# Kernel optimization log

Hardware: AMD Instinct MI355X
Metric: run time of the kernel (lower is better)

The kernel has to match this reference:

```python
import jax, jax.numpy as jnp
import numpy as np

N_GRAPHS = 1000
P = 300                 # nodes per ring graph
N = N_GRAPHS * P        # 300000 nodes
IN_DIM = 2
HID = 128
OUT_DIM = 2


def _ring_edges():
    idx = jnp.arange(N)
    g = idx // P
    pos = idx % P
    nxt = g * P + (pos + 1) % P
    src = jnp.concatenate([idx, nxt])
    dst = jnp.concatenate([nxt, idx])
    return jnp.stack([src, dst]), g


def setup_inputs() -> dict:
    key = jax.random.key(0)
    ks = jax.random.split(key, 11)
    edge_index, batch = _ring_edges()
    x = jax.random.normal(ks[0], (N, IN_DIM), jnp.float32)

    def glorot(k, fan_in, fan_out):
        lim = np.sqrt(6.0 / (fan_in + fan_out)).astype(np.float32)
        return jax.random.uniform(k, (fan_in, fan_out), jnp.float32, -lim, lim)

    return {
        "x": x,
        "edge_index": edge_index,
        "batch": batch,
        "W1": glorot(ks[1], IN_DIM, HID), "b1": jnp.zeros((HID,), jnp.float32),
        "W2": glorot(ks[2], HID, HID),    "b2": jnp.zeros((HID,), jnp.float32),
        "W3": glorot(ks[3], HID, HID),    "b3": jnp.zeros((HID,), jnp.float32),
        "fw1": glorot(ks[4], HID, HID),   "fb1": jnp.zeros((HID,), jnp.float32),
        "fw2": glorot(ks[5], HID, OUT_DIM), "fb2": jnp.zeros((OUT_DIM,), jnp.float32),
    }


def _gcn_conv(x, W, b, src, dst, norm):
    h = x @ W                              # [N, out]
    msg = h[src] * norm[:, None]           # gather + per-edge scale
    agg = jax.ops.segment_sum(msg, dst, num_segments=N)  # scatter-add
    return agg + b


def reference(x, edge_index, batch, W1, b1, W2, b2, W3, b3, fw1, fb1, fw2, fb2):
    loop = jnp.arange(N)
    src = jnp.concatenate([edge_index[0], loop])
    dst = jnp.concatenate([edge_index[1], loop])
    deg = jax.ops.segment_sum(jnp.ones_like(dst, jnp.float32), dst, num_segments=N)
    dis = jax.lax.rsqrt(deg)               # deg >= 1 due to self-loops
    norm = dis[src] * dis[dst]             # per-edge normalization

    h = jax.nn.relu(_gcn_conv(x, W1, b1, src, dst, norm))
    h = jax.nn.relu(_gcn_conv(h, W2, b2, src, dst, norm))
    h = jax.nn.relu(_gcn_conv(h, W3, b3, src, dst, norm))

    # global mean pool per graph
    sums = jax.ops.segment_sum(h, batch, num_segments=N_GRAPHS)
    cnts = jax.ops.segment_sum(jnp.ones((N,), jnp.float32), batch, num_segments=N_GRAPHS)
    pooled = sums / cnts[:, None]

    out = jax.nn.relu(pooled @ fw1 + fb1)
    out = out @ fw2 + fb2
    return out
```

## Files before the change

### kernel.cpp

```cpp
#include <hip/hip_runtime.h>
#include <hip/hip_bf16.h>
#include <stdint.h>

#define P    300
#define HID  128
#define NG   1000
#define NTL  19

typedef __attribute__((ext_vector_type(8))) short bf16x8;
typedef __attribute__((ext_vector_type(4))) float f32x4;

__device__ short g_wsw[2 * HID * HID];

__device__ __forceinline__ short f2bf(float f) {
    union { float f; uint32_t u; } v; v.f = f;
    uint32_t r = v.u + 0x7fffu + ((v.u >> 16) & 1u);
    return (short)(r >> 16);
}
__device__ __forceinline__ float bf2f(short s) {
    union { uint32_t u; float f; } v; v.u = ((uint32_t)(uint16_t)s) << 16;
    return v.f;
}
__device__ __forceinline__ uint32_t pkbf2(float a, float b) {
    union { __hip_bfloat162 h; uint32_t u; } cv;
    cv.h = __float22bfloat162_rn(float2{a, b});
    return cv.u;
}
__device__ __forceinline__ float unpk(int v, int ft) {
    return bf2f((short)(ft ? (((uint32_t)v) >> 16) : (v & 0xffff)));
}

__global__ __launch_bounds__(256) void k_prep(const float* __restrict__ W2,
                                              const float* __restrict__ W3) {
    int b = blockIdx.x;
    const bool perm = (b < 8);
    const float* W = perm ? W2 : W3;
    short* dst = g_wsw + (perm ? 0 : HID * HID);
    int t    = (b & 7) * 256 + threadIdx.x;
    int fkey = t >> 4;
    int kc   = t & 15;
    int fsrc;
    if (perm) {
        int u = fkey >> 5, ft = (fkey >> 4) & 1, l = fkey & 15;
        fsrc = u * 32 + 2 * l + ft;
    } else fsrc = fkey;
    bf16x8 o;
    #pragma unroll
    for (int j = 0; j < 8; ++j)
        o[j] = f2bf(W[(kc * 8 + j) * HID + fsrc]);
    *(bf16x8*)&dst[(fkey * 16 + (kc ^ (fkey & 15))) * 8] = o;
}

__device__ __forceinline__ void avg_epi(const float* G, float vp0, float vn3,
                                        float b, float* o) {
    o[0] = (vp0  + G[0] + G[1]) * (1.0f / 3.0f) + b;
    o[1] = (G[0] + G[1] + G[2]) * (1.0f / 3.0f) + b;
    o[2] = (G[1] + G[2] + G[3]) * (1.0f / 3.0f) + b;
    o[3] = (G[2] + G[3] + vn3 ) * (1.0f / 3.0f) + b;
    #pragma unroll
    for (int i = 0; i < 4; ++i) o[i] = o[i] > 0.f ? o[i] : 0.f;
}

template<int POOL>
__device__ __forceinline__ void run_pass(short* __restrict__ buf,
                                         const short* __restrict__ wbase,
                                         const float* __restrict__ bias,
                                         float* __restrict__ pool, int tid) {
    const int lane = tid & 63, wv = tid >> 6, q = lane >> 4, lm = lane & 15;
    const int ftg0 = wv * 2;
    bf16x8 wf[2][4];
    #pragma unroll
    for (int ft = 0; ft < 2; ++ft) {
        int fkey = (ftg0 + ft) * 16 + lm;
        #pragma unroll
        for (int kk = 0; kk < 4; ++kk)
            wf[ft][kk] = *(const bf16x8*)&wbase[(fkey * 16 + ((4 * kk + q) ^ lm)) * 8];
    }
    float biaf[2];
    #pragma unroll
    for (int ft = 0; ft < 2; ++ft)
        biaf[ft] = POOL ? bias[(ftg0 + ft) * 16 + lm] : bias[wv * 32 + 2 * lm + ft];
    const int sA = (q == 0) ? (48 + lm) : (lane - 16);
    const int sB = (lane + 16) & 63;
    const int fpair = wv * 32 + 2 * lm;
    const int kcs = fpair >> 3, offs = fpair & 7;

    float psum[2] = {0.f, 0.f};

    auto mfma_tile = [&](int t, f32x4* G) {
        const short* tb = buf + t * 2048;
        G[0] = f32x4{0.f, 0.f, 0.f, 0.f};
        G[1] = f32x4{0.f, 0.f, 0.f, 0.f};
        #pragma unroll
        for (int kk = 0; kk < 4; ++kk) {
            bf16x8 af = *(const bf16x8*)&tb[(lm * 16 + ((4 * kk + q) ^ lm)) * 8];
            G[0] = __builtin_amdgcn_mfma_f32_16x16x32_bf16(af, wf[0][kk], G[0], 0, 0, 0);
            G[1] = __builtin_amdgcn_mfma_f32_16x16x32_bf16(af, wf[1][kk], G[1], 0, 0, 0);
        }
    };
    auto store_rows = [&](int T, float (&o)[2][4]) {
        #pragma unroll
        for (int i = 0; i < 4; ++i) {
            int node = T * 16 + q * 4 + i;
            *(uint32_t*)&buf[(node * 16 + (kcs ^ (node & 15))) * 8 + offs] =
                pkbf2(o[0][i], o[1][i]);
        }
    };
    auto accum = [&](float (&o)[2][4]) {
        #pragma unroll
        for (int ft = 0; ft < 2; ++ft)
            psum[ft] += o[ft][0] + o[ft][1] + o[ft][2] + o[ft][3];
    };

    float c15[2];
    auto epi_mid = [&](const f32x4 (&E)[2], uint32_t uN0, float (&o)[2][4]) {
        uint32_t uE3 = pkbf2(E[0][3], E[1][3]);
        uint32_t uE0 = pkbf2(E[0][0], E[1][0]);
        int vA = __shfl((int)uE3, sA, 64);
        int vB = __shfl((int)uE0, sB, 64);
        int vC = __shfl((int)uN0, lm, 64);
        #pragma unroll
        for (int ft = 0; ft < 2; ++ft) {
            float bpA = unpk(vA, ft);
            float vp0 = (q == 0) ? c15[ft] : bpA;
            float vn3 = (q == 3) ? unpk(vC, ft) : unpk(vB, ft);
            avg_epi((const float*)&E[ft], vp0, vn3, biaf[ft], o[ft]);
            c15[ft] = bpA;
        }
    };

    f32x4 GH[10][2];
    f32x4 GL[9][2];

    #pragma unroll
    for (int k = 0; k < 9; ++k) mfma_tile(10 + k, GH[k]);
    mfma_tile(0, GH[9]);
    if (!POOL) __syncthreads();

    #pragma unroll
    for (int i = 0; i < 9; ++i) {
        mfma_tile(9 - i, GL[i]);
        if (i == 0) {
            int v = __shfl((int)pkbf2(GL[0][0][3], GL[0][1][3]), 48 + lm, 64);
            c15[0] = unpk(v, 0); c15[1] = unpk(v, 1);
        }
        if (i < 8) {
            float o[2][4];
            uint32_t uN0 = pkbf2(GH[i + 1][0][0], GH[i + 1][1][0]);
            epi_mid(GH[i], uN0, o);
            if (POOL) accum(o); else store_rows(10 + i, o);
        } else {
            float o18[2][4];
            uint32_t uE3 = pkbf2(GH[8][0][3], GH[8][1][3]);
            uint32_t uE0 = pkbf2(GH[8][0][0], GH[8][1][0]);
            uint32_t uZ0 = pkbf2(GH[9][0][0], GH[9][1][0]);
            int vA = __shfl((int)uE3, sA, 64);
            int vB = __shfl((int)uE0, sB, 64);
            int vZ = __shfl((int)uZ0, lm, 64);
            #pragma unroll
            for (int ft = 0; ft < 2; ++ft) {
                float bpA = unpk(vA, ft);
                float vp0 = (q == 0) ? c15[ft] : bpA;
                float vn3 = (q == 2) ? unpk(vZ, ft) : unpk(vB, ft);
                avg_epi((const float*)&GH[8][ft], vp0, vn3, biaf[ft], o18[ft]);
            }
            if (q < 3) { if (POOL) accum(o18); else store_rows(18, o18); }
            float o0[2][4];
            uint32_t uF3 = pkbf2(GH[9][0][3], GH[9][1][3]);
            int vA0 = __shfl((int)uF3, (lane - 16) & 63, 64);
            int vB0 = __shfl((int)uZ0, sB, 64);
            int vP  = __shfl((int)uE3, 32 + lm, 64);
            uint32_t uG1 = pkbf2(GL[8][0][0], GL[8][1][0]);
            int vN = __shfl((int)uG1, lm, 64);
            #pragma unroll
            for (int ft = 0; ft < 2; ++ft) {
                float vp0 = (q == 0) ? unpk(vP, ft) : unpk(vA0, ft);
                float vn3 = (q == 3) ? unpk(vN, ft) : unpk(vB0, ft);
                avg_epi((const float*)&GH[9][ft], vp0, vn3, biaf[ft], o0[ft]);
            }
            if (POOL) accum(o0); else store_rows(0, o0);
        }
    }
    if (!POOL) __syncthreads();

    {
        int v = __shfl((int)pkbf2(GH[9][0][3], GH[9][1][3]), 48 + lm, 64);
        c15[0] = unpk(v, 0); c15[1] = unpk(v, 1);
    }
    #pragma unroll
    for (int T = 1; T <= 9; ++T) {
        float o[2][4];
        uint32_t uN0 = (T < 9) ? pkbf2(GL[8 - T][0][0], GL[8 - T][1][0])
                               : pkbf2(GH[0][0][0], GH[0][1][0]);
        epi_mid(GL[9 - T], uN0, o);
        if (POOL) accum(o); else store_rows(T, o);
    }

    if (POOL) {
        #pragma unroll
        for (int ft = 0; ft < 2; ++ft) {
            psum[ft] += __shfl_xor(psum[ft], 16, 64);
            psum[ft] += __shfl_xor(psum[ft], 32, 64);
        }
        if (q == 0) {
            pool[ftg0 * 16 + lm]      = psum[0];
            pool[ftg0 * 16 + 16 + lm] = psum[1];
        }
    }
}

__global__ __launch_bounds__(256, 2) void k_graph(
        const float* __restrict__ x,
        const float* __restrict__ W1,  const float* __restrict__ b1,
        const float* __restrict__ b2v, const float* __restrict__ b3v,
        const float* __restrict__ fw1, const float* __restrict__ fb1,
        const float* __restrict__ fw2, const float* __restrict__ fb2,
        float* __restrict__ out) {
    __shared__ __align__(16) short buf[304 * HID];
    __shared__ __align__(16) float scr[640];
    float* xs    = scr;
    float* pool  = scr;
    float* parts = scr + 128;
    float* s1    = scr + 384;

    const int g = blockIdx.x, tid = threadIdx.x;

    if (tid < 150) *(float4*)&xs[tid * 4] = *(const float4*)&x[g * 600 + tid * 4];
    __syncthreads();

    {
        const int kc1 = tid & 15;
        const int n0  = tid >> 4;
        float w1x[8], w1y[8], b1v[8];
        #pragma unroll
        for (int j = 0; j < 8; ++j) {
            w1x[j] = W1[kc1 * 8 + j];
            w1y[j] = W1[HID + kc1 * 8 + j];
            b1v[j] = b1[kc1 * 8 + j];
        }
        #pragma unroll
        for (int it = 0; it < NTL; ++it) {
            int node = it * 16 + n0;
            uint32_t w[4] = {0u, 0u, 0u, 0u};
            if (node < P) {
                int prev = (node == 0)     ? P - 1 : node - 1;
                int next = (node == P - 1) ? 0     : node + 1;
                float2 xp = *(const float2*)&xs[2 * prev];
                float2 xc = *(const float2*)&xs[2 * node];
                float2 xn = *(const float2*)&xs[2 * next];
                float ax = (xp.x + xc.x + xn.x) * (1.f / 3.f);
                float ay = (xp.y + xc.y + xn.y) * (1.f / 3.f);
                #pragma unroll
                for (int jj = 0; jj < 4; ++jj) {
                    float va = ax * w1x[2*jj]   + ay * w1y[2*jj]   + b1v[2*jj];
                    float vb = ax * w1x[2*jj+1] + ay * w1y[2*jj+1] + b1v[2*jj+1];
                    va = va > 0.f ? va : 0.f;
                    vb = vb > 0.f ? vb : 0.f;
                    w[jj] = pkbf2(va, vb);
                }
            }
            *(uint4*)&buf[(node * 16 + (kc1 ^ (node & 15))) * 8] =
                uint4{w[0], w[1], w[2], w[3]};
        }
    }
    __syncthreads();

    run_pass<0>(buf, g_wsw,             b2v, pool, tid);
    __syncthreads();
    run_pass<1>(buf, g_wsw + HID * HID, b3v, pool, tid);
    __syncthreads();

    {
        int f = tid & 127, half = tid >> 7;
        float p = 0.f;
        const float* fw1c = fw1 + f;
        #pragma unroll 4
        for (int k = half * 64; k < half * 64 + 64; ++k)
            p += pool[k] * fw1c[k * 128];
        parts[half * 128 + f] = p;
    }
    __syncthreads();
    if (tid < 128) {
        float o1 = fb1[tid] + (parts[tid] + parts[128 + tid]) * (1.0f / 300.0f);
        s1[tid] = o1 > 0.f ? o1 : 0.f;
    }
    __syncthreads();
    if (tid < 128) {
        int o = tid >> 6, ln = tid & 63;
        float v = s1[ln] * fw2[ln * 2 + o] + s1[ln + 64] * fw2[(ln + 64) * 2 + o];
        #pragma unroll
        for (int off = 1; off <= 32; off <<= 1)
            v += __shfl_xor(v, off, 64);
        if (ln == 0) out[g * 2 + o] = v + fb2[o];
    }
}

extern "C" void kernel_launch(void* const* d_in, const int* in_sizes, int n_in,
                              void* d_out, int out_size, void* d_ws, size_t ws_size,
                              hipStream_t stream) {
    const float* x   = (const float*)d_in[0];
    const float* W1  = (const float*)d_in[3];
    const float* b1  = (const float*)d_in[4];
    const float* W2  = (const float*)d_in[5];
    const float* b2  = (const float*)d_in[6];
    const float* W3  = (const float*)d_in[7];
    const float* b3  = (const float*)d_in[8];
    const float* fw1 = (const float*)d_in[9];
    const float* fb1 = (const float*)d_in[10];
    const float* fw2 = (const float*)d_in[11];
    const float* fb2 = (const float*)d_in[12];
    float* out = (float*)d_out;

    k_prep <<<dim3(16), dim3(256), 0, stream>>>(W2, W3);
    k_graph<<<dim3(NG), dim3(256), 0, stream>>>(x, W1, b1, b2, b3,
                                                fw1, fb1, fw2, fb2, out);
}
```

Measured before the change: 123.3 us.

## Replace cross-lane shuffle neighbor exchange with small shift-matrix MFMAs

The ring-neighbor averaging epilogue used to move boundary rows between lanes with several __shfl calls per tile and bf16 unpacking. It now packs every tile's accumulator to bf16 once and feeds the packed values to 16x16x16 MFMAs against constant shift/selection matrices, which bring the cross-row (and wrap-around) neighbor values into each lane's accumulator. This moves the lane exchange from LDS-backed shuffles onto the matrix units. In exchange it adds extra MFMAs per tile and a 19x2 array of packed bf16 tiles that raises register pressure, which may cause spills or lower occupancy.

```diff
diff --git a/kernel.cpp b/kernel.cpp
--- a/kernel.cpp
+++ b/kernel.cpp
@@ -8,6 +8,7 @@
 #define NTL  19
 
 typedef __attribute__((ext_vector_type(8))) short bf16x8;
+typedef __attribute__((ext_vector_type(4))) short bf16x4;
 typedef __attribute__((ext_vector_type(4))) float f32x4;
 
 __device__ short g_wsw[2 * HID * HID];
@@ -17,17 +18,19 @@
     uint32_t r = v.u + 0x7fffu + ((v.u >> 16) & 1u);
     return (short)(r >> 16);
 }
-__device__ __forceinline__ float bf2f(short s) {
-    union { uint32_t u; float f; } v; v.u = ((uint32_t)(uint16_t)s) << 16;
-    return v.f;
-}
 __device__ __forceinline__ uint32_t pkbf2(float a, float b) {
     union { __hip_bfloat162 h; uint32_t u; } cv;
     cv.h = __float22bfloat162_rn(float2{a, b});
     return cv.u;
 }
-__device__ __forceinline__ float unpk(int v, int ft) {
-    return bf2f((short)(ft ? (((uint32_t)v) >> 16) : (v & 0xffff)));
+
+__device__ __forceinline__ f32x4 mfma16(bf16x4 a, bf16x4 b, f32x4 c) {
+#if __has_builtin(__builtin_amdgcn_mfma_f32_16x16x16bf16_1k)
+    return __builtin_amdgcn_mfma_f32_16x16x16bf16_1k(a, b, c, 0, 0, 0);
+#else
+    asm("v_mfma_f32_16x16x16_bf16 %0, %1, %2, %0" : "+v"(c) : "v"(a), "v"(b));
+    return c;
+#endif
 }
 
 __global__ __launch_bounds__(256) void k_prep(const float* __restrict__ W2,
@@ -51,16 +54,6 @@
     *(bf16x8*)&dst[(fkey * 16 + (kc ^ (fkey & 15))) * 8] = o;
 }
 
-__device__ __forceinline__ void avg_epi(const float* G, float vp0, float vn3,
-                                        float b, float* o) {
-    o[0] = (vp0  + G[0] + G[1]) * (1.0f / 3.0f) + b;
-    o[1] = (G[0] + G[1] + G[2]) * (1.0f / 3.0f) + b;
-    o[2] = (G[1] + G[2] + G[3]) * (1.0f / 3.0f) + b;
-    o[3] = (G[2] + G[3] + vn3 ) * (1.0f / 3.0f) + b;
-    #pragma unroll
-    for (int i = 0; i < 4; ++i) o[i] = o[i] > 0.f ? o[i] : 0.f;
-}
-
 template<int POOL>
 __device__ __forceinline__ void run_pass(short* __restrict__ buf,
                                          const short* __restrict__ wbase,
@@ -80,12 +73,25 @@
     #pragma unroll
     for (int ft = 0; ft < 2; ++ft)
         biaf[ft] = POOL ? bias[(ftg0 + ft) * 16 + lm] : bias[wv * 32 + 2 * lm + ft];
-    const int sA = (q == 0) ? (48 + lm) : (lane - 16);
-    const int sB = (lane + 16) & 63;
     const int fpair = wv * 32 + 2 * lm;
     const int kcs = fpair >> 3, offs = fpair & 7;
 
+    const short ONE = (short)0x3F80;
+    bf16x4 Sb = {0, 0, 0, 0}, Sp = {0, 0, 0, 0}, Sn = {0, 0, 0, 0},
+           Swa = {0, 0, 0, 0}, Swb = {0, 0, 0, 0};
+    #pragma unroll
+    for (int j = 0; j < 4; ++j) {
+        const int k = 4 * q + j;
+        if (((lm & 3) == 0 && k == lm - 1) || ((lm & 3) == 3 && k == lm + 1))
+            Sb[j] = ONE;
+        if (lm == 0  && k == 15) Sp[j]  = ONE;
+        if (lm == 15 && k == 0 ) Sn[j]  = ONE;
+        if (lm == 11 && k == 0 ) Swa[j] = ONE;
+        if (lm == 0  && k == 11) Swb[j] = ONE;
+    }
+
     float psum[2] = {0.f, 0.f};
+    bf16x4 bq[NTL][2];
 
     auto mfma_tile = [&](int t, f32x4* G) {
         const short* tb = buf + t * 2048;
@@ -112,20 +118,31 @@
             psum[ft] += o[ft][0] + o[ft][1] + o[ft][2] + o[ft][3];
     };
 
-    float c15[2];
-    auto epi_mid = [&](const f32x4 (&E)[2], uint32_t uN0, float (&o)[2][4]) {
-        uint32_t uE3 = pkbf2(E[0][3], E[1][3]);
-        uint32_t uE0 = pkbf2(E[0][0], E[1][0]);
-        int vA = __shfl((int)uE3, sA, 64);
-        int vB = __shfl((int)uE0, sB, 64);
-        int vC = __shfl((int)uN0, lm, 64);
+    auto epi = [&](const f32x4 (&E)[2], const bf16x4 (&bT)[2],
+                   const bf16x4 (&bP)[2], const bf16x4 (&bN)[2],
+                   int wrap, float (&o)[2][4]) {
         #pragma unroll
         for (int ft = 0; ft < 2; ++ft) {
-            float bpA = unpk(vA, ft);
-            float vp0 = (q == 0) ? c15[ft] : bpA;
-            float vn3 = (q == 3) ? unpk(vC, ft) : unpk(vB, ft);
-            avg_epi((const float*)&E[ft], vp0, vn3, biaf[ft], o[ft]);
-            c15[ft] = bpA;
+            f32x4 C = {0.f, 0.f, 0.f, 0.f};
+            C = mfma16(Sb, bT[ft], C);
+            C = mfma16(Sp, bP[ft], C);
+            C = mfma16(Sn, bN[ft], C);
+            if (wrap == 1) C = mfma16(Swa, bq[0][ft], C);
+            if (wrap == 2) C = mfma16(Swb, bq[18][ft], C);
+            const float s0 = E[ft][0] + E[ft][1];
+            const float s2 = E[ft][2] + E[ft][3];
+            float t0 = C[0] + s0;
+            float t1 = s0 + E[ft][2];
+            float t2 = E[ft][1] + s2;
+            float t3 = s2 + C[3];
+            float v0 = fmaf(t0, 1.f / 3.f, biaf[ft]);
+            float v1 = fmaf(t1, 1.f / 3.f, biaf[ft]);
+            float v2 = fmaf(t2, 1.f / 3.f, biaf[ft]);
+            float v3 = fmaf(t3, 1.f / 3.f, biaf[ft]);
+            o[ft][0] = v0 > 0.f ? v0 : 0.f;
+            o[ft][1] = v1 > 0.f ? v1 : 0.f;
+            o[ft][2] = v2 > 0.f ? v2 : 0.f;
+            o[ft][3] = v3 > 0.f ? v3 : 0.f;
         }
     };
 
@@ -133,66 +150,55 @@
     f32x4 GL[9][2];
 
     #pragma unroll
-    for (int k = 0; k < 9; ++k) mfma_tile(10 + k, GH[k]);
+    for (int k = 0; k < 9; ++k) {
+        mfma_tile(10 + k, GH[k]);
+        #pragma unroll
+        for (int ft = 0; ft < 2; ++ft) {
+            union { bf16x4 v; uint32_t u[2]; } pk;
+            pk.u[0] = pkbf2(GH[k][ft][0], GH[k][ft][1]);
+            pk.u[1] = pkbf2(GH[k][ft][2], GH[k][ft][3]);
+            bq[10 + k][ft] = pk.v;
+        }
+    }
     mfma_tile(0, GH[9]);
+    #pragma unroll
+    for (int ft = 0; ft < 2; ++ft) {
+        union { bf16x4 v; uint32_t u[2]; } pk;
+        pk.u[0] = pkbf2(GH[9][ft][0], GH[9][ft][1]);
+        pk.u[1] = pkbf2(GH[9][ft][2], GH[9][ft][3]);
+        bq[0][ft] = pk.v;
+    }
     if (!POOL) __syncthreads();
 
     #pragma unroll
     for (int i = 0; i < 9; ++i) {
         mfma_tile(9 - i, GL[i]);
-        if (i == 0) {
-            int v = __shfl((int)pkbf2(GL[0][0][3], GL[0][1][3]), 48 + lm, 64);
-            c15[0] = unpk(v, 0); c15[1] = unpk(v, 1);
+        #pragma unroll
+        for (int ft = 0; ft < 2; ++ft) {
+            union { bf16x4 v; uint32_t u[2]; } pk;
+            pk.u[0] = pkbf2(GL[i][ft][0], GL[i][ft][1]);
+            pk.u[1] = pkbf2(GL[i][ft][2], GL[i][ft][3]);
+            bq[9 - i][ft] = pk.v;
         }
         if (i < 8) {
             float o[2][4];
-            uint32_t uN0 = pkbf2(GH[i + 1][0][0], GH[i + 1][1][0]);
-            epi_mid(GH[i], uN0, o);
+            epi(GH[i], bq[10 + i], bq[9 + i], bq[11 + i], 0, o);
             if (POOL) accum(o); else store_rows(10 + i, o);
         } else {
             float o18[2][4];
-            uint32_t uE3 = pkbf2(GH[8][0][3], GH[8][1][3]);
-            uint32_t uE0 = pkbf2(GH[8][0][0], GH[8][1][0]);
-            uint32_t uZ0 = pkbf2(GH[9][0][0], GH[9][1][0]);
-            int vA = __shfl((int)uE3, sA, 64);
-            int vB = __shfl((int)uE0, sB, 64);
-            int vZ = __shfl((int)uZ0, lm, 64);
-            #pragma unroll
-            for (int ft = 0; ft < 2; ++ft) {
-                float bpA = unpk(vA, ft);
-                float vp0 = (q == 0) ? c15[ft] : bpA;
-                float vn3 = (q == 2) ? unpk(vZ, ft) : unpk(vB, ft);
-                avg_epi((const float*)&GH[8][ft], vp0, vn3, biaf[ft], o18[ft]);
-            }
+            epi(GH[8], bq[18], bq[17], bq[0], 1, o18);
             if (q < 3) { if (POOL) accum(o18); else store_rows(18, o18); }
             float o0[2][4];
-            uint32_t uF3 = pkbf2(GH[9][0][3], GH[9][1][3]);
-            int vA0 = __shfl((int)uF3, (lane - 16) & 63, 64);
-            int vB0 = __shfl((int)uZ0, sB, 64);
-            int vP  = __shfl((int)uE3, 32 + lm, 64);
-            uint32_t uG1 = pkbf2(GL[8][0][0], GL[8][1][0]);
-            int vN = __shfl((int)uG1, lm, 64);
-            #pragma unroll
-            for (int ft = 0; ft < 2; ++ft) {
-                float vp0 = (q == 0) ? unpk(vP, ft) : unpk(vA0, ft);
-                float vn3 = (q == 3) ? unpk(vN, ft) : unpk(vB0, ft);
-                avg_epi((const float*)&GH[9][ft], vp0, vn3, biaf[ft], o0[ft]);
-            }
+            epi(GH[9], bq[0], bq[18], bq[1], 2, o0);
             if (POOL) accum(o0); else store_rows(0, o0);
         }
     }
     if (!POOL) __syncthreads();
 
-    {
-        int v = __shfl((int)pkbf2(GH[9][0][3], GH[9][1][3]), 48 + lm, 64);
-        c15[0] = unpk(v, 0); c15[1] = unpk(v, 1);
-    }
     #pragma unroll
     for (int T = 1; T <= 9; ++T) {
         float o[2][4];
-        uint32_t uN0 = (T < 9) ? pkbf2(GL[8 - T][0][0], GL[8 - T][1][0])
-                               : pkbf2(GH[0][0][0], GH[0][1][0]);
-        epi_mid(GL[9 - T], uN0, o);
+        epi(GL[9 - T], bq[T], bq[T - 1], bq[T + 1], 0, o);
         if (POOL) accum(o); else store_rows(T, o);
     }
 
```

New measurement: 132.6 us. 1.08x slower.

## Split each ring graph across four blocks with halo rows and separate FC kernel

Applied to the files above, without the earlier changes.

Each graph is now handled by four blocks, each owning 75 nodes plus a 3-node halo on both sides, so the grid grows from 1000 to 4000 blocks. Shared memory per block shrinks from 304 to 80 rows, which should raise occupancy and improve load balance across CUs. The halo rows are recomputed redundantly, and only interior rows are stored or pooled. Partial pool sums go to a global buffer that a new third kernel reduces before running the FC head. This adds a kernel launch and a global round trip for the pooled features.

```diff
diff --git a/kernel.cpp b/kernel.cpp
--- a/kernel.cpp
+++ b/kernel.cpp
@@ -5,12 +5,13 @@
 #define P    300
 #define HID  128
 #define NG   1000
-#define NTL  19
+#define QR   80
 
 typedef __attribute__((ext_vector_type(8))) short bf16x8;
 typedef __attribute__((ext_vector_type(4))) float f32x4;
 
 __device__ short g_wsw[2 * HID * HID];
+__device__ float g_pool[NG * 4 * HID];
 
 __device__ __forceinline__ short f2bf(float f) {
     union { float f; uint32_t u; } v; v.f = f;
@@ -51,7 +52,7 @@
     *(bf16x8*)&dst[(fkey * 16 + (kc ^ (fkey & 15))) * 8] = o;
 }
 
-__device__ __forceinline__ void avg_epi(const float* G, float vp0, float vn3,
+__device__ __forceinline__ void avg_epi(const f32x4 &G, float vp0, float vn3,
                                         float b, float* o) {
     o[0] = (vp0  + G[0] + G[1]) * (1.0f / 3.0f) + b;
     o[1] = (G[0] + G[1] + G[2]) * (1.0f / 3.0f) + b;
@@ -61,7 +62,7 @@
     for (int i = 0; i < 4; ++i) o[i] = o[i] > 0.f ? o[i] : 0.f;
 }
 
-template<int POOL>
+template<int POOL, int LO, int HI>
 __device__ __forceinline__ void run_pass(short* __restrict__ buf,
                                          const short* __restrict__ wbase,
                                          const float* __restrict__ bias,
@@ -80,14 +81,15 @@
     #pragma unroll
     for (int ft = 0; ft < 2; ++ft)
         biaf[ft] = POOL ? bias[(ftg0 + ft) * 16 + lm] : bias[wv * 32 + 2 * lm + ft];
+    const int fpair = wv * 32 + 2 * lm;
+    const int kcs = fpair >> 3, offs = fpair & 7;
     const int sA = (q == 0) ? (48 + lm) : (lane - 16);
     const int sB = (lane + 16) & 63;
-    const int fpair = wv * 32 + 2 * lm;
-    const int kcs = fpair >> 3, offs = fpair & 7;
 
     float psum[2] = {0.f, 0.f};
-
-    auto mfma_tile = [&](int t, f32x4* G) {
+    float c15[2] = {0.f, 0.f};
+
+    auto mfma_tile = [&](int t, f32x4 (&G)[2]) {
         const short* tb = buf + t * 2048;
         G[0] = f32x4{0.f, 0.f, 0.f, 0.f};
         G[1] = f32x4{0.f, 0.f, 0.f, 0.f};
@@ -101,21 +103,23 @@
     auto store_rows = [&](int T, float (&o)[2][4]) {
         #pragma unroll
         for (int i = 0; i < 4; ++i) {
-            int node = T * 16 + q * 4 + i;
-            *(uint32_t*)&buf[(node * 16 + (kcs ^ (node & 15))) * 8 + offs] =
-                pkbf2(o[0][i], o[1][i]);
-        }
-    };
-    auto accum = [&](float (&o)[2][4]) {
-        #pragma unroll
-        for (int ft = 0; ft < 2; ++ft)
-            psum[ft] += o[ft][0] + o[ft][1] + o[ft][2] + o[ft][3];
-    };
-
-    float c15[2];
-    auto epi_mid = [&](const f32x4 (&E)[2], uint32_t uN0, float (&o)[2][4]) {
+            int r = T * 16 + q * 4 + i;
+            if (r >= LO && r <= HI)
+                *(uint32_t*)&buf[(r * 16 + (kcs ^ (r & 15))) * 8 + offs] =
+                    pkbf2(o[0][i], o[1][i]);
+        }
+    };
+    auto accum = [&](int T, float (&o)[2][4]) {
+        #pragma unroll
+        for (int i = 0; i < 4; ++i) {
+            int r = T * 16 + q * 4 + i;
+            if (r >= LO && r <= HI) { psum[0] += o[0][i]; psum[1] += o[1][i]; }
+        }
+    };
+    auto epi = [&](const f32x4 (&E)[2], const f32x4 (&N)[2], float (&o)[2][4]) {
         uint32_t uE3 = pkbf2(E[0][3], E[1][3]);
         uint32_t uE0 = pkbf2(E[0][0], E[1][0]);
+        uint32_t uN0 = pkbf2(N[0][0], N[1][0]);
         int vA = __shfl((int)uE3, sA, 64);
         int vB = __shfl((int)uE0, sB, 64);
         int vC = __shfl((int)uN0, lm, 64);
@@ -124,76 +128,46 @@
             float bpA = unpk(vA, ft);
             float vp0 = (q == 0) ? c15[ft] : bpA;
             float vn3 = (q == 3) ? unpk(vC, ft) : unpk(vB, ft);
-            avg_epi((const float*)&E[ft], vp0, vn3, biaf[ft], o[ft]);
+            avg_epi(E[ft], vp0, vn3, biaf[ft], o[ft]);
             c15[ft] = bpA;
         }
     };
 
-    f32x4 GH[10][2];
-    f32x4 GL[9][2];
-
-    #pragma unroll
-    for (int k = 0; k < 9; ++k) mfma_tile(10 + k, GH[k]);
-    mfma_tile(0, GH[9]);
+    f32x4 Ga[2], Gb[2], Gc[2], Gd[2], Ge[2];
+
+    mfma_tile(0, Ga);
+    mfma_tile(1, Gb);
+    mfma_tile(2, Gc);
     if (!POOL) __syncthreads();
 
-    #pragma unroll
-    for (int i = 0; i < 9; ++i) {
-        mfma_tile(9 - i, GL[i]);
-        if (i == 0) {
-            int v = __shfl((int)pkbf2(GL[0][0][3], GL[0][1][3]), 48 + lm, 64);
-            c15[0] = unpk(v, 0); c15[1] = unpk(v, 1);
-        }
-        if (i < 8) {
-            float o[2][4];
-            uint32_t uN0 = pkbf2(GH[i + 1][0][0], GH[i + 1][1][0]);
-            epi_mid(GH[i], uN0, o);
-            if (POOL) accum(o); else store_rows(10 + i, o);
-        } else {
-            float o18[2][4];
-            uint32_t uE3 = pkbf2(GH[8][0][3], GH[8][1][3]);
-            uint32_t uE0 = pkbf2(GH[8][0][0], GH[8][1][0]);
-            uint32_t uZ0 = pkbf2(GH[9][0][0], GH[9][1][0]);
-            int vA = __shfl((int)uE3, sA, 64);
-            int vB = __shfl((int)uE0, sB, 64);
-            int vZ = __shfl((int)uZ0, lm, 64);
-            #pragma unroll
-            for (int ft = 0; ft < 2; ++ft) {
-                float bpA = unpk(vA, ft);
-                float vp0 = (q == 0) ? c15[ft] : bpA;
-                float vn3 = (q == 2) ? unpk(vZ, ft) : unpk(vB, ft);
-                avg_epi((const float*)&GH[8][ft], vp0, vn3, biaf[ft], o18[ft]);
-            }
-            if (q < 3) { if (POOL) accum(o18); else store_rows(18, o18); }
-            float o0[2][4];
-            uint32_t uF3 = pkbf2(GH[9][0][3], GH[9][1][3]);
-            int vA0 = __shfl((int)uF3, (lane - 16) & 63, 64);
-            int vB0 = __shfl((int)uZ0, sB, 64);
-            int vP  = __shfl((int)uE3, 32 + lm, 64);
-            uint32_t uG1 = pkbf2(GL[8][0][0], GL[8][1][0]);
-            int vN = __shfl((int)uG1, lm, 64);
-            #pragma unroll
-            for (int ft = 0; ft < 2; ++ft) {
-                float vp0 = (q == 0) ? unpk(vP, ft) : unpk(vA0, ft);
-                float vn3 = (q == 3) ? unpk(vN, ft) : unpk(vB0, ft);
-                avg_epi((const float*)&GH[9][ft], vp0, vn3, biaf[ft], o0[ft]);
-            }
-            if (POOL) accum(o0); else store_rows(0, o0);
-        }
+    mfma_tile(3, Gd);
+    {
+        float o[2][4];
+        epi(Ga, Gb, o);
+        if (POOL) accum(0, o); else store_rows(0, o);
+    }
+    mfma_tile(4, Ge);
+    {
+        float o[2][4];
+        epi(Gb, Gc, o);
+        if (POOL) accum(1, o); else store_rows(1, o);
     }
     if (!POOL) __syncthreads();
 
     {
-        int v = __shfl((int)pkbf2(GH[9][0][3], GH[9][1][3]), 48 + lm, 64);
-        c15[0] = unpk(v, 0); c15[1] = unpk(v, 1);
-    }
-    #pragma unroll
-    for (int T = 1; T <= 9; ++T) {
-        float o[2][4];
-        uint32_t uN0 = (T < 9) ? pkbf2(GL[8 - T][0][0], GL[8 - T][1][0])
-                               : pkbf2(GH[0][0][0], GH[0][1][0]);
-        epi_mid(GL[9 - T], uN0, o);
-        if (POOL) accum(o); else store_rows(T, o);
+        float o[2][4];
+        epi(Gc, Gd, o);
+        if (POOL) accum(2, o); else store_rows(2, o);
+    }
+    {
+        float o[2][4];
+        epi(Gd, Ge, o);
+        if (POOL) accum(3, o); else store_rows(3, o);
+    }
+    {
+        float o[2][4];
+        epi(Ge, Ge, o);
+        if (POOL) accum(4, o); else store_rows(4, o);
     }
 
     if (POOL) {
@@ -203,8 +177,8 @@
             psum[ft] += __shfl_xor(psum[ft], 32, 64);
         }
         if (q == 0) {
-            pool[ftg0 * 16 + lm]      = psum[0];
-            pool[ftg0 * 16 + 16 + lm] = psum[1];
+            pool[ftg0 * 16 + lm]        = psum[0];
+            pool[(ftg0 + 1) * 16 + lm]  = psum[1];
         }
     }
 }
@@ -212,20 +186,19 @@
 __global__ __launch_bounds__(256, 2) void k_graph(
         const float* __restrict__ x,
         const float* __restrict__ W1,  const float* __restrict__ b1,
-        const float* __restrict__ b2v, const float* __restrict__ b3v,
-        const float* __restrict__ fw1, const float* __restrict__ fb1,
-        const float* __restrict__ fw2, const float* __restrict__ fb2,
-        float* __restrict__ out) {
-    __shared__ __align__(16) short buf[304 * HID];
-    __shared__ __align__(16) float scr[640];
-    float* xs    = scr;
-    float* pool  = scr;
-    float* parts = scr + 128;
-    float* s1    = scr + 384;
-
-    const int g = blockIdx.x, tid = threadIdx.x;
-
-    if (tid < 150) *(float4*)&xs[tid * 4] = *(const float4*)&x[g * 600 + tid * 4];
+        const float* __restrict__ b2v, const float* __restrict__ b3v) {
+    __shared__ __align__(16) short buf[QR * HID];
+    __shared__ __align__(16) float xs[164];
+    const int bid = blockIdx.x, g = bid >> 2, qt = bid & 3;
+    const int tid = threadIdx.x;
+    const int start = qt * 75;
+
+    if (tid < 81) {
+        int gn = start - 3 + tid;
+        gn += (gn < 0) ? P : 0;
+        gn -= (gn >= P) ? P : 0;
+        *(float2*)&xs[2 * tid] = *(const float2*)&x[g * 600 + gn * 2];
+    }
     __syncthreads();
 
     {
@@ -239,15 +212,13 @@
             b1v[j] = b1[kc1 * 8 + j];
         }
         #pragma unroll
-        for (int it = 0; it < NTL; ++it) {
-            int node = it * 16 + n0;
+        for (int it = 0; it < 5; ++it) {
+            int row = it * 16 + n0;
             uint32_t w[4] = {0u, 0u, 0u, 0u};
-            if (node < P) {
-                int prev = (node == 0)     ? P - 1 : node - 1;
-                int next = (node == P - 1) ? 0     : node + 1;
-                float2 xp = *(const float2*)&xs[2 * prev];
-                float2 xc = *(const float2*)&xs[2 * node];
-                float2 xn = *(const float2*)&xs[2 * next];
+            if (row < 79) {
+                float2 xp = *(const float2*)&xs[2 * row];
+                float2 xc = *(const float2*)&xs[2 * row + 2];
+                float2 xn = *(const float2*)&xs[2 * row + 4];
                 float ax = (xp.x + xc.x + xn.x) * (1.f / 3.f);
                 float ay = (xp.y + xc.y + xn.y) * (1.f / 3.f);
                 #pragma unroll
@@ -259,40 +230,40 @@
                     w[jj] = pkbf2(va, vb);
                 }
             }
-            *(uint4*)&buf[(node * 16 + (kc1 ^ (node & 15))) * 8] =
+            *(uint4*)&buf[(row * 16 + (kc1 ^ (row & 15))) * 8] =
                 uint4{w[0], w[1], w[2], w[3]};
         }
     }
     __syncthreads();
 
-    run_pass<0>(buf, g_wsw,             b2v, pool, tid);
-    __syncthreads();
-    run_pass<1>(buf, g_wsw + HID * HID, b3v, pool, tid);
-    __syncthreads();
-
-    {
-        int f = tid & 127, half = tid >> 7;
-        float p = 0.f;
-        const float* fw1c = fw1 + f;
-        #pragma unroll 4
-        for (int k = half * 64; k < half * 64 + 64; ++k)
-            p += pool[k] * fw1c[k * 128];
-        parts[half * 128 + f] = p;
-    }
-    __syncthreads();
-    if (tid < 128) {
-        float o1 = fb1[tid] + (parts[tid] + parts[128 + tid]) * (1.0f / 300.0f);
-        s1[tid] = o1 > 0.f ? o1 : 0.f;
-    }
-    __syncthreads();
-    if (tid < 128) {
-        int o = tid >> 6, ln = tid & 63;
-        float v = s1[ln] * fw2[ln * 2 + o] + s1[ln + 64] * fw2[(ln + 64) * 2 + o];
-        #pragma unroll
-        for (int off = 1; off <= 32; off <<= 1)
-            v += __shfl_xor(v, off, 64);
-        if (ln == 0) out[g * 2 + o] = v + fb2[o];
-    }
+    run_pass<0, 1, 77>(buf, g_wsw,             b2v, nullptr, tid);
+    __syncthreads();
+    run_pass<1, 2, 76>(buf, g_wsw + HID * HID, b3v,
+                       &g_pool[(g * 4 + qt) * HID], tid);
+}
+
+__global__ __launch_bounds__(128) void k_fc(
+        const float* __restrict__ fw1, const float* __restrict__ fb1,
+        const float* __restrict__ fw2, const float* __restrict__ fb2,
+        float* __restrict__ out) {
+    __shared__ float pl[128], s1[128];
+    const int g = blockIdx.x, f = threadIdx.x;
+    pl[f] = g_pool[g * 512 + f]       + g_pool[g * 512 + 128 + f]
+          + g_pool[g * 512 + 256 + f] + g_pool[g * 512 + 384 + f];
+    __syncthreads();
+    float p = 0.f;
+    const float* c = fw1 + f;
+    #pragma unroll 8
+    for (int k = 0; k < 128; ++k) p += pl[k] * c[k * 128];
+    float o1 = fb1[f] + p * (1.0f / 300.0f);
+    s1[f] = o1 > 0.f ? o1 : 0.f;
+    __syncthreads();
+    int o = f >> 6, ln = f & 63;
+    float v = s1[ln] * fw2[ln * 2 + o] + s1[ln + 64] * fw2[(ln + 64) * 2 + o];
+    #pragma unroll
+    for (int off = 1; off <= 32; off <<= 1)
+        v += __shfl_xor(v, off, 64);
+    if (ln == 0) out[g * 2 + o] = v + fb2[o];
 }
 
 extern "C" void kernel_launch(void* const* d_in, const int* in_sizes, int n_in,
@@ -311,7 +282,7 @@
     const float* fb2 = (const float*)d_in[12];
     float* out = (float*)d_out;
 
-    k_prep <<<dim3(16), dim3(256), 0, stream>>>(W2, W3);
-    k_graph<<<dim3(NG), dim3(256), 0, stream>>>(x, W1, b1, b2, b3,
-                                                fw1, fb1, fw2, fb2, out);
-}
+    k_prep <<<dim3(16),     dim3(256), 0, stream>>>(W2, W3);
+    k_graph<<<dim3(4 * NG), dim3(256), 0, stream>>>(x, W1, b1, b2, b3);
+    k_fc   <<<dim3(NG),     dim3(128), 0, stream>>>(fw1, fb1, fw2, fb2, out);
+}
```

Measured after the change: 127.6 us. +3.5%, slower.
